# Optimization experiments

Measured on AMD Instinct MI355X. Metric: run time of the kernel, lower is better.

## Reference

```python
import jax, jax.numpy as jnp
import numpy as np

EF_DIM = 128
KNN_NUM = 8
N_POINTS = 100000


def setup_inputs() -> dict:
    key = jax.random.key(0)
    k1, k2, k3, k4, k5, k6, k7 = jax.random.split(key, 7)
    inp = jax.random.normal(k1, (N_POINTS, EF_DIM), dtype=jnp.float32)
    knn_idx = jax.random.randint(k2, (N_POINTS * KNN_NUM,), 0, N_POINTS, dtype=jnp.int64)
    knn_xyz = jax.random.normal(k3, (N_POINTS * KNN_NUM, 3), dtype=jnp.float32)
    # Linear params (stored as [in, out] so y = x @ W + b, same math as torch Linear)
    s1 = 1.0 / np.sqrt(EF_DIM + 3)
    s2 = 1.0 / np.sqrt(EF_DIM)
    W1 = jax.random.uniform(k4, (EF_DIM + 3, EF_DIM), minval=-s1, maxval=s1, dtype=jnp.float32)
    b1 = jax.random.uniform(k5, (EF_DIM,), minval=-s1, maxval=s1, dtype=jnp.float32)
    W2 = jax.random.uniform(k6, (EF_DIM, EF_DIM), minval=-s2, maxval=s2, dtype=jnp.float32)
    b2 = jax.random.uniform(k7, (EF_DIM,), minval=-s2, maxval=s2, dtype=jnp.float32)
    return {"input": inp, "KNN_idx": knn_idx, "KNN_xyz": knn_xyz,
            "W1": W1, "b1": b1, "W2": W2, "b2": b2}


def reference(input, KNN_idx, KNN_xyz, W1, b1, W2, b2):
    # Gather neighbor features: [N*K, ef_dim]
    gathered = input[KNN_idx]
    # Concat relative xyz: [N*K, ef_dim + 3]
    h = jnp.concatenate([gathered, KNN_xyz], axis=1)
    h = h @ W1 + b1
    h = jax.nn.leaky_relu(h, negative_slope=0.01)
    h = h @ W2 + b2
    # Max-pool over the KNN dimension: [N, ef_dim]
    h = h.reshape(-1, KNN_NUM, EF_DIM)
    return jnp.max(h, axis=1)
```

## Files before the change

### kernel.cpp

```cpp
#include <hip/hip_runtime.h>
#include <hip/hip_bf16.h>

#define EF 128
#define KNN 8

typedef __attribute__((ext_vector_type(8)))  short          short8;
typedef __attribute__((ext_vector_type(8)))  unsigned short ushort8;
typedef __attribute__((ext_vector_type(4)))  float          f32x4;
typedef __attribute__((ext_vector_type(16))) float          f32x16;

static __device__ __forceinline__ unsigned short f2bf(float f) {
    unsigned int x = __float_as_uint(f);
    unsigned int r = x + 0x7fffu + ((x >> 16) & 1u);
    return (unsigned short)(r >> 16);
}
static __device__ __forceinline__ short f2bf_hw(float f) {
    return (short)__bfloat16_as_ushort(__float2bfloat16(f));
}

__global__ __launch_bounds__(256) void pack_kernel(
    const float* __restrict__ W1, const float* __restrict__ W2,
    unsigned short* __restrict__ W1p, unsigned short* __restrict__ W2p)
{
    int t = blockIdx.x * 256 + threadIdx.x;
    if (t < 16384) {
        int s = t;
        int j  = s & 7;
        int l  = (s >> 3) & 63;
        int nt = (s >> 9) & 3;
        int kt = (s >> 11) & 7;
        int k = kt * 16 + (l >> 5) * 8 + j;
        int n = nt * 32 + (l & 31);
        W1p[s] = f2bf(W1[k * EF + n]);
    } else if (t < 32768) {
        int s = t - 16384;
        int j  = s & 7;
        int l  = (s >> 3) & 63;
        int nt = (s >> 9) & 7;
        int kt = (s >> 12) & 3;
        int k = kt * 32 + (l >> 4) * 8 + j;
        int n = nt * 16 + (l & 15);
        W2p[s] = f2bf(W2[k * EF + n]);
    }
}

__global__ __launch_bounds__(256) void zgemm_kernel(
    const float* __restrict__ input,
    const unsigned short* __restrict__ W1p,
    const float* __restrict__ b1,
    unsigned short* __restrict__ Z,
    int npts, int ntiles)
{
    int l = threadIdx.x & 63;
    int tile = blockIdx.x * 4 + (threadIdx.x >> 6);
    if (tile >= ntiles) return;
    int p0   = tile * 32;
    int r    = l & 31;
    int half = l >> 5;
    int prow = p0 + r;
    if (prow >= npts) prow = npts - 1;
    const float* Arow = input + (size_t)prow * EF;

    f32x16 acc[4];
#pragma unroll
    for (int nt = 0; nt < 4; ++nt)
#pragma unroll
        for (int i = 0; i < 16; ++i) acc[nt][i] = 0.f;

#pragma unroll
    for (int kt = 0; kt < 8; ++kt) {
        int k0 = kt * 16 + half * 8;
        float4 a0 = *(const float4*)(Arow + k0);
        float4 a1 = *(const float4*)(Arow + k0 + 4);
        short8 a;
        a[0] = f2bf_hw(a0.x); a[1] = f2bf_hw(a0.y);
        a[2] = f2bf_hw(a0.z); a[3] = f2bf_hw(a0.w);
        a[4] = f2bf_hw(a1.x); a[5] = f2bf_hw(a1.y);
        a[6] = f2bf_hw(a1.z); a[7] = f2bf_hw(a1.w);
#pragma unroll
        for (int nt = 0; nt < 4; ++nt) {
            short8 b = *(const short8*)(W1p + ((size_t)((kt * 4 + nt) * 64 + l)) * 8);
            acc[nt] = __builtin_amdgcn_mfma_f32_32x32x16_bf16(a, b, acc[nt], 0, 0, 0);
        }
    }

    int col = l & 31;
#pragma unroll
    for (int nt = 0; nt < 4; ++nt) {
        float bb = b1[nt * 32 + col];
#pragma unroll
        for (int reg = 0; reg < 16; ++reg) {
            int row = (reg & 3) + 8 * (reg >> 2) + 4 * half;
            int p = p0 + row;
            if (p < npts)
                Z[(size_t)p * EF + nt * 32 + col] = f2bf(acc[nt][reg] + bb);
        }
    }
}

__global__ __launch_bounds__(512) void edge_mfma_kernel(
    const unsigned short* __restrict__ Z,
    const int* __restrict__ knn_idx,
    const float* __restrict__ knn_xyz,
    const unsigned short* __restrict__ W2p,
    const float* __restrict__ W1,
    const float* __restrict__ b2,
    float* __restrict__ out,
    int npts, int nedges, int ntiles)
{
    __shared__ short8 w2lds[2048];
    __shared__ float  wlds[3 * EF];

    int l    = threadIdx.x & 63;
    int tile = blockIdx.x * 8 + (threadIdx.x >> 6);
    bool active = tile < ntiles;

    int E0 = tile * 16;
    int r  = l & 15;
    int hi = l >> 4;
    int edge = active ? (E0 + r) : 0;
    if (edge >= nedges) edge = nedges - 1;

    int   idx = knn_idx[edge];
    float x = knn_xyz[edge * 3 + 0];
    float y = knn_xyz[edge * 3 + 1];
    float z = knn_xyz[edge * 3 + 2];
    const unsigned short* Zrow = Z + (size_t)idx * EF;
    ushort8 zv[4];
#pragma unroll
    for (int kt = 0; kt < 4; ++kt)
        zv[kt] = *(const ushort8*)(Zrow + kt * 32 + hi * 8);

    {
        const short8* W2v = (const short8*)W2p;
#pragma unroll
        for (int i = threadIdx.x; i < 2048; i += 512)
            w2lds[i] = W2v[i];
        for (int t = threadIdx.x; t < 3 * EF; t += 512)
            wlds[t] = W1[EF * EF + t];
    }
    __syncthreads();
    if (!active) return;

    f32x4 acc[8];
#pragma unroll
    for (int nt = 0; nt < 8; ++nt)
#pragma unroll
        for (int i = 0; i < 4; ++i) acc[nt][i] = 0.f;

#pragma unroll
    for (int kt = 0; kt < 4; ++kt) {
        int d0 = kt * 32 + hi * 8;
        float4 wx0 = *(const float4*)&wlds[0 * EF + d0];
        float4 wx1 = *(const float4*)&wlds[0 * EF + d0 + 4];
        float4 wy0 = *(const float4*)&wlds[1 * EF + d0];
        float4 wy1 = *(const float4*)&wlds[1 * EF + d0 + 4];
        float4 wz0 = *(const float4*)&wlds[2 * EF + d0];
        float4 wz1 = *(const float4*)&wlds[2 * EF + d0 + 4];
        float wxa[8] = {wx0.x, wx0.y, wx0.z, wx0.w, wx1.x, wx1.y, wx1.z, wx1.w};
        float wya[8] = {wy0.x, wy0.y, wy0.z, wy0.w, wy1.x, wy1.y, wy1.z, wy1.w};
        float wza[8] = {wz0.x, wz0.y, wz0.z, wz0.w, wz1.x, wz1.y, wz1.z, wz1.w};

        short8 a;
#pragma unroll
        for (int j = 0; j < 8; ++j) {
            float h = __uint_as_float(((unsigned int)zv[kt][j]) << 16);
            h = fmaf(x, wxa[j], h);
            h = fmaf(y, wya[j], h);
            h = fmaf(z, wza[j], h);
            h = fmaxf(h, 0.01f * h);
            a[j] = f2bf_hw(h);
        }
#pragma unroll
        for (int nt = 0; nt < 8; ++nt) {
            short8 b = w2lds[(kt * 8 + nt) * 64 + l];
            acc[nt] = __builtin_amdgcn_mfma_f32_16x16x32_bf16(a, b, acc[nt], 0, 0, 0);
        }
    }

    int col = l & 15;
#pragma unroll
    for (int nt = 0; nt < 8; ++nt) {
        float m = fmaxf(fmaxf(acc[nt][0], acc[nt][1]),
                        fmaxf(acc[nt][2], acc[nt][3]));
        m = fmaxf(m, __shfl_xor(m, 16));
        if (!(hi & 1)) {
            int p = tile * 2 + (hi >> 1);
            if (p < npts)
                out[(size_t)p * EF + nt * 16 + col] = m + b2[nt * 16 + col];
        }
    }
}

extern "C" void kernel_launch(void* const* d_in, const int* in_sizes, int n_in,
                              void* d_out, int out_size, void* d_ws, size_t ws_size,
                              hipStream_t stream) {
    const float* input   = (const float*)d_in[0];
    const int*   knn_idx = (const int*)  d_in[1];
    const float* knn_xyz = (const float*)d_in[2];
    const float* W1      = (const float*)d_in[3];
    const float* b1      = (const float*)d_in[4];
    const float* W2      = (const float*)d_in[5];
    const float* b2      = (const float*)d_in[6];
    float*       out     = (float*)d_out;

    int npts   = in_sizes[0] / EF;
    int nedges = in_sizes[1];

    unsigned short* W1p = (unsigned short*)d_ws;
    unsigned short* W2p = W1p + 16384;
    unsigned short* Z   = (unsigned short*)((char*)d_ws + 65536);

    pack_kernel<<<128, 256, 0, stream>>>(W1, W2, W1p, W2p);

    int ztiles = (npts + 31) / 32;
    zgemm_kernel<<<(ztiles + 3) / 4, 256, 0, stream>>>(
        input, W1p, b1, Z, npts, ztiles);

    int etiles = (nedges + 15) / 16;
    edge_mfma_kernel<<<(etiles + 7) / 8, 512, 0, stream>>>(
        Z, knn_idx, knn_xyz, W2p, W1, b2, out, npts, nedges, etiles);
}
```

Baseline: 91.96 us.

## Make edge kernel persistent with double-buffered gather prefetch

The edge kernel now runs a capped grid of 1024 blocks. Each wave loops over tiles with a grid stride and prefetches the next tile's neighbor Z rows and xyz into registers while it computes the current tile. This spreads the W2/W1 LDS staging over many tiles and hides gather latency behind the MFMA work. The cost is higher register pressure from the two buffers, which may lower occupancy, and fewer waves available for latency hiding.

```diff
diff --git a/kernel.cpp b/kernel.cpp
--- a/kernel.cpp
+++ b/kernel.cpp
@@ -111,26 +111,6 @@
     __shared__ short8 w2lds[2048];
     __shared__ float  wlds[3 * EF];
 
-    int l    = threadIdx.x & 63;
-    int tile = blockIdx.x * 8 + (threadIdx.x >> 6);
-    bool active = tile < ntiles;
-
-    int E0 = tile * 16;
-    int r  = l & 15;
-    int hi = l >> 4;
-    int edge = active ? (E0 + r) : 0;
-    if (edge >= nedges) edge = nedges - 1;
-
-    int   idx = knn_idx[edge];
-    float x = knn_xyz[edge * 3 + 0];
-    float y = knn_xyz[edge * 3 + 1];
-    float z = knn_xyz[edge * 3 + 2];
-    const unsigned short* Zrow = Z + (size_t)idx * EF;
-    ushort8 zv[4];
-#pragma unroll
-    for (int kt = 0; kt < 4; ++kt)
-        zv[kt] = *(const ushort8*)(Zrow + kt * 32 + hi * 8);
-
     {
         const short8* W2v = (const short8*)W2p;
 #pragma unroll
@@ -140,55 +120,96 @@
             wlds[t] = W1[EF * EF + t];
     }
     __syncthreads();
-    if (!active) return;
-
-    f32x4 acc[8];
-#pragma unroll
-    for (int nt = 0; nt < 8; ++nt)
-#pragma unroll
-        for (int i = 0; i < 4; ++i) acc[nt][i] = 0.f;
-
-#pragma unroll
-    for (int kt = 0; kt < 4; ++kt) {
-        int d0 = kt * 32 + hi * 8;
-        float4 wx0 = *(const float4*)&wlds[0 * EF + d0];
-        float4 wx1 = *(const float4*)&wlds[0 * EF + d0 + 4];
-        float4 wy0 = *(const float4*)&wlds[1 * EF + d0];
-        float4 wy1 = *(const float4*)&wlds[1 * EF + d0 + 4];
-        float4 wz0 = *(const float4*)&wlds[2 * EF + d0];
-        float4 wz1 = *(const float4*)&wlds[2 * EF + d0 + 4];
-        float wxa[8] = {wx0.x, wx0.y, wx0.z, wx0.w, wx1.x, wx1.y, wx1.z, wx1.w};
-        float wya[8] = {wy0.x, wy0.y, wy0.z, wy0.w, wy1.x, wy1.y, wy1.z, wy1.w};
-        float wza[8] = {wz0.x, wz0.y, wz0.z, wz0.w, wz1.x, wz1.y, wz1.z, wz1.w};
-
-        short8 a;
-#pragma unroll
-        for (int j = 0; j < 8; ++j) {
-            float h = __uint_as_float(((unsigned int)zv[kt][j]) << 16);
-            h = fmaf(x, wxa[j], h);
-            h = fmaf(y, wya[j], h);
-            h = fmaf(z, wza[j], h);
-            h = fmaxf(h, 0.01f * h);
-            a[j] = f2bf_hw(h);
-        }
+
+    int l  = threadIdx.x & 63;
+    int r  = l & 15;
+    int hi = l >> 4;
+    int wid    = blockIdx.x * 8 + (threadIdx.x >> 6);
+    int stride = gridDim.x * 8;
+
+    ushort8 zvA[4], zvB[4];
+    float xA, yA, zA, xB, yB, zB;
+
+    auto fetch = [&](int tile, ushort8 (&zv)[4], float& x, float& y, float& z) {
+        int edge = tile * 16 + r;
+        if (edge >= nedges) edge = nedges - 1;
+        int idx = knn_idx[edge];
+        x = knn_xyz[edge * 3 + 0];
+        y = knn_xyz[edge * 3 + 1];
+        z = knn_xyz[edge * 3 + 2];
+        const unsigned short* Zrow = Z + (size_t)idx * EF;
+#pragma unroll
+        for (int kt = 0; kt < 4; ++kt)
+            zv[kt] = *(const ushort8*)(Zrow + kt * 32 + hi * 8);
+    };
+
+    auto compute = [&](int tile, const ushort8 (&zv)[4],
+                       float x, float y, float z) {
+        f32x4 acc[8];
+#pragma unroll
+        for (int nt = 0; nt < 8; ++nt)
+#pragma unroll
+            for (int i = 0; i < 4; ++i) acc[nt][i] = 0.f;
+
+#pragma unroll
+        for (int kt = 0; kt < 4; ++kt) {
+            int d0 = kt * 32 + hi * 8;
+            float4 wx0 = *(const float4*)&wlds[0 * EF + d0];
+            float4 wx1 = *(const float4*)&wlds[0 * EF + d0 + 4];
+            float4 wy0 = *(const float4*)&wlds[1 * EF + d0];
+            float4 wy1 = *(const float4*)&wlds[1 * EF + d0 + 4];
+            float4 wz0 = *(const float4*)&wlds[2 * EF + d0];
+            float4 wz1 = *(const float4*)&wlds[2 * EF + d0 + 4];
+            float wxa[8] = {wx0.x, wx0.y, wx0.z, wx0.w, wx1.x, wx1.y, wx1.z, wx1.w};
+            float wya[8] = {wy0.x, wy0.y, wy0.z, wy0.w, wy1.x, wy1.y, wy1.z, wy1.w};
+            float wza[8] = {wz0.x, wz0.y, wz0.z, wz0.w, wz1.x, wz1.y, wz1.z, wz1.w};
+
+            short8 a;
+#pragma unroll
+            for (int j = 0; j < 8; ++j) {
+                float h = __uint_as_float(((unsigned int)zv[kt][j]) << 16);
+                h = fmaf(x, wxa[j], h);
+                h = fmaf(y, wya[j], h);
+                h = fmaf(z, wza[j], h);
+                h = fmaxf(h, 0.01f * h);
+                a[j] = f2bf_hw(h);
+            }
+#pragma unroll
+            for (int nt = 0; nt < 8; ++nt) {
+                short8 b = w2lds[(kt * 8 + nt) * 64 + l];
+                acc[nt] = __builtin_amdgcn_mfma_f32_16x16x32_bf16(a, b, acc[nt], 0, 0, 0);
+            }
+        }
+
+        int col = l & 15;
 #pragma unroll
         for (int nt = 0; nt < 8; ++nt) {
-            short8 b = w2lds[(kt * 8 + nt) * 64 + l];
-            acc[nt] = __builtin_amdgcn_mfma_f32_16x16x32_bf16(a, b, acc[nt], 0, 0, 0);
-        }
-    }
-
-    int col = l & 15;
-#pragma unroll
-    for (int nt = 0; nt < 8; ++nt) {
-        float m = fmaxf(fmaxf(acc[nt][0], acc[nt][1]),
-                        fmaxf(acc[nt][2], acc[nt][3]));
-        m = fmaxf(m, __shfl_xor(m, 16));
-        if (!(hi & 1)) {
-            int p = tile * 2 + (hi >> 1);
-            if (p < npts)
-                out[(size_t)p * EF + nt * 16 + col] = m + b2[nt * 16 + col];
-        }
+            float m = fmaxf(fmaxf(acc[nt][0], acc[nt][1]),
+                            fmaxf(acc[nt][2], acc[nt][3]));
+            m = fmaxf(m, __shfl_xor(m, 16));
+            if (!(hi & 1)) {
+                int p = tile * 2 + (hi >> 1);
+                if (p < npts)
+                    out[(size_t)p * EF + nt * 16 + col] = m + b2[nt * 16 + col];
+            }
+        }
+    };
+
+    int t = wid;
+    if (t >= ntiles) return;
+    fetch(t, zvA, xA, yA, zA);
+    while (true) {
+        int tn = t + stride;
+        bool more = tn < ntiles;
+        if (more) fetch(tn, zvB, xB, yB, zB);
+        compute(t, zvA, xA, yA, zA);
+        if (!more) break;
+        int tnn = tn + stride;
+        bool more2 = tnn < ntiles;
+        if (more2) fetch(tnn, zvA, xA, yA, zA);
+        compute(tn, zvB, xB, yB, zB);
+        if (!more2) break;
+        t = tnn;
     }
 }
 
@@ -218,6 +239,8 @@
         input, W1p, b1, Z, npts, ztiles);
 
     int etiles = (nedges + 15) / 16;
-    edge_mfma_kernel<<<(etiles + 7) / 8, 512, 0, stream>>>(
+    int eblocks = (etiles + 7) / 8;
+    if (eblocks > 1024) eblocks = 1024;
+    edge_mfma_kernel<<<eblocks, 512, 0, stream>>>(
         Z, knn_idx, knn_xyz, W2p, W1, b2, out, npts, nedges, etiles);
 }
```

Result: slower. 235.6 us (+156.2%).

## Process two edge tiles per wave and keep xyz weights in registers as bf16

Applied to the files above, without the earlier changes.

Each wave in the edge kernel now handles 32 edges (two 16-edge MFMA tiles) instead of 16. This halves the number of blocks and reuses each W2 LDS fragment for two MFMAs. The xyz rows of W1 are no longer staged through LDS; each lane loads them from global memory and keeps them in registers as packed bf16. The W2 LDS fill is issued before the gathers so the loads can overlap. In exchange, register pressure rises (two accumulator sets), which may lower occupancy, and rounding the xyz weights to bf16 slightly changes numerics.

```diff
diff --git a/kernel.cpp b/kernel.cpp
--- a/kernel.cpp
+++ b/kernel.cpp
@@ -16,6 +16,10 @@
 }
 static __device__ __forceinline__ short f2bf_hw(float f) {
     return (short)__bfloat16_as_ushort(__float2bfloat16(f));
+}
+static __device__ __forceinline__ unsigned int pk2bf(float a, float b) {
+    return (unsigned int)(unsigned short)f2bf_hw(a)
+         | ((unsigned int)(unsigned short)f2bf_hw(b) << 16);
 }
 
 __global__ __launch_bounds__(256) void pack_kernel(
@@ -109,85 +113,125 @@
     int npts, int nedges, int ntiles)
 {
     __shared__ short8 w2lds[2048];
-    __shared__ float  wlds[3 * EF];
-
-    int l    = threadIdx.x & 63;
+
+    {
+        const short8* W2v = (const short8*)W2p;
+#pragma unroll
+        for (int i = threadIdx.x; i < 2048; i += 512)
+            w2lds[i] = W2v[i];
+    }
+
+    int l  = threadIdx.x & 63;
+    int r  = l & 15;
+    int hi = l >> 4;
     int tile = blockIdx.x * 8 + (threadIdx.x >> 6);
     bool active = tile < ntiles;
 
-    int E0 = tile * 16;
-    int r  = l & 15;
-    int hi = l >> 4;
-    int edge = active ? (E0 + r) : 0;
-    if (edge >= nedges) edge = nedges - 1;
-
-    int   idx = knn_idx[edge];
-    float x = knn_xyz[edge * 3 + 0];
-    float y = knn_xyz[edge * 3 + 1];
-    float z = knn_xyz[edge * 3 + 2];
-    const unsigned short* Zrow = Z + (size_t)idx * EF;
-    ushort8 zv[4];
-#pragma unroll
-    for (int kt = 0; kt < 4; ++kt)
-        zv[kt] = *(const ushort8*)(Zrow + kt * 32 + hi * 8);
-
+    unsigned int wxp[4][4], wyp[4][4], wzp[4][4];
     {
-        const short8* W2v = (const short8*)W2p;
-#pragma unroll
-        for (int i = threadIdx.x; i < 2048; i += 512)
-            w2lds[i] = W2v[i];
-        for (int t = threadIdx.x; t < 3 * EF; t += 512)
-            wlds[t] = W1[EF * EF + t];
-    }
+        const float* W1x = W1 + EF * EF;
+#pragma unroll
+        for (int kt = 0; kt < 4; ++kt) {
+            int d0 = kt * 32 + hi * 8;
+            float4 xa = *(const float4*)(W1x + 0 * EF + d0);
+            float4 xb = *(const float4*)(W1x + 0 * EF + d0 + 4);
+            float4 ya = *(const float4*)(W1x + 1 * EF + d0);
+            float4 yb = *(const float4*)(W1x + 1 * EF + d0 + 4);
+            float4 za = *(const float4*)(W1x + 2 * EF + d0);
+            float4 zb = *(const float4*)(W1x + 2 * EF + d0 + 4);
+            wxp[kt][0] = pk2bf(xa.x, xa.y); wxp[kt][1] = pk2bf(xa.z, xa.w);
+            wxp[kt][2] = pk2bf(xb.x, xb.y); wxp[kt][3] = pk2bf(xb.z, xb.w);
+            wyp[kt][0] = pk2bf(ya.x, ya.y); wyp[kt][1] = pk2bf(ya.z, ya.w);
+            wyp[kt][2] = pk2bf(yb.x, yb.y); wyp[kt][3] = pk2bf(yb.z, yb.w);
+            wzp[kt][0] = pk2bf(za.x, za.y); wzp[kt][1] = pk2bf(za.z, za.w);
+            wzp[kt][2] = pk2bf(zb.x, zb.y); wzp[kt][3] = pk2bf(zb.z, zb.w);
+        }
+    }
+
+    int eA = tile * 32 + r;
+    int eB = tile * 32 + 16 + r;
+    if (!active) { eA = 0; eB = 0; }
+    if (eA >= nedges) eA = nedges - 1;
+    if (eB >= nedges) eB = nedges - 1;
+
+    int   iA = knn_idx[eA],            iB = knn_idx[eB];
+    float xA = knn_xyz[eA * 3 + 0],    xB = knn_xyz[eB * 3 + 0];
+    float yA = knn_xyz[eA * 3 + 1],    yB = knn_xyz[eB * 3 + 1];
+    float zA = knn_xyz[eA * 3 + 2],    zB = knn_xyz[eB * 3 + 2];
+    const unsigned short* ZrA = Z + (size_t)iA * EF;
+    const unsigned short* ZrB = Z + (size_t)iB * EF;
+
+    ushort8 zvA[4], zvB[4];
+#pragma unroll
+    for (int kt = 0; kt < 4; ++kt) {
+        zvA[kt] = *(const ushort8*)(ZrA + kt * 32 + hi * 8);
+        zvB[kt] = *(const ushort8*)(ZrB + kt * 32 + hi * 8);
+    }
+
     __syncthreads();
     if (!active) return;
 
-    f32x4 acc[8];
+    f32x4 acc0[8], acc1[8];
 #pragma unroll
     for (int nt = 0; nt < 8; ++nt)
 #pragma unroll
-        for (int i = 0; i < 4; ++i) acc[nt][i] = 0.f;
+        for (int i = 0; i < 4; ++i) { acc0[nt][i] = 0.f; acc1[nt][i] = 0.f; }
 
 #pragma unroll
     for (int kt = 0; kt < 4; ++kt) {
-        int d0 = kt * 32 + hi * 8;
-        float4 wx0 = *(const float4*)&wlds[0 * EF + d0];
-        float4 wx1 = *(const float4*)&wlds[0 * EF + d0 + 4];
-        float4 wy0 = *(const float4*)&wlds[1 * EF + d0];
-        float4 wy1 = *(const float4*)&wlds[1 * EF + d0 + 4];
-        float4 wz0 = *(const float4*)&wlds[2 * EF + d0];
-        float4 wz1 = *(const float4*)&wlds[2 * EF + d0 + 4];
-        float wxa[8] = {wx0.x, wx0.y, wx0.z, wx0.w, wx1.x, wx1.y, wx1.z, wx1.w};
-        float wya[8] = {wy0.x, wy0.y, wy0.z, wy0.w, wy1.x, wy1.y, wy1.z, wy1.w};
-        float wza[8] = {wz0.x, wz0.y, wz0.z, wz0.w, wz1.x, wz1.y, wz1.z, wz1.w};
-
-        short8 a;
-#pragma unroll
-        for (int j = 0; j < 8; ++j) {
-            float h = __uint_as_float(((unsigned int)zv[kt][j]) << 16);
-            h = fmaf(x, wxa[j], h);
-            h = fmaf(y, wya[j], h);
-            h = fmaf(z, wza[j], h);
-            h = fmaxf(h, 0.01f * h);
-            a[j] = f2bf_hw(h);
+        short8 a0, a1;
+#pragma unroll
+        for (int jj = 0; jj < 4; ++jj) {
+            unsigned int wxu = wxp[kt][jj];
+            unsigned int wyu = wyp[kt][jj];
+            unsigned int wzu = wzp[kt][jj];
+            float wx0 = __uint_as_float(wxu << 16);
+            float wx1 = __uint_as_float(wxu & 0xffff0000u);
+            float wy0 = __uint_as_float(wyu << 16);
+            float wy1 = __uint_as_float(wyu & 0xffff0000u);
+            float wz0 = __uint_as_float(wzu << 16);
+            float wz1 = __uint_as_float(wzu & 0xffff0000u);
+
+            float h0 = __uint_as_float(((unsigned int)zvA[kt][2 * jj + 0]) << 16);
+            float h1 = __uint_as_float(((unsigned int)zvA[kt][2 * jj + 1]) << 16);
+            h0 = fmaf(xA, wx0, h0); h1 = fmaf(xA, wx1, h1);
+            h0 = fmaf(yA, wy0, h0); h1 = fmaf(yA, wy1, h1);
+            h0 = fmaf(zA, wz0, h0); h1 = fmaf(zA, wz1, h1);
+            h0 = fmaxf(h0, 0.01f * h0); h1 = fmaxf(h1, 0.01f * h1);
+            a0[2 * jj + 0] = f2bf_hw(h0); a0[2 * jj + 1] = f2bf_hw(h1);
+
+            float g0 = __uint_as_float(((unsigned int)zvB[kt][2 * jj + 0]) << 16);
+            float g1 = __uint_as_float(((unsigned int)zvB[kt][2 * jj + 1]) << 16);
+            g0 = fmaf(xB, wx0, g0); g1 = fmaf(xB, wx1, g1);
+            g0 = fmaf(yB, wy0, g0); g1 = fmaf(yB, wy1, g1);
+            g0 = fmaf(zB, wz0, g0); g1 = fmaf(zB, wz1, g1);
+            g0 = fmaxf(g0, 0.01f * g0); g1 = fmaxf(g1, 0.01f * g1);
+            a1[2 * jj + 0] = f2bf_hw(g0); a1[2 * jj + 1] = f2bf_hw(g1);
         }
 #pragma unroll
         for (int nt = 0; nt < 8; ++nt) {
             short8 b = w2lds[(kt * 8 + nt) * 64 + l];
-            acc[nt] = __builtin_amdgcn_mfma_f32_16x16x32_bf16(a, b, acc[nt], 0, 0, 0);
+            acc0[nt] = __builtin_amdgcn_mfma_f32_16x16x32_bf16(a0, b, acc0[nt], 0, 0, 0);
+            acc1[nt] = __builtin_amdgcn_mfma_f32_16x16x32_bf16(a1, b, acc1[nt], 0, 0, 0);
         }
     }
 
     int col = l & 15;
+    int p0  = tile * 4;
 #pragma unroll
     for (int nt = 0; nt < 8; ++nt) {
-        float m = fmaxf(fmaxf(acc[nt][0], acc[nt][1]),
-                        fmaxf(acc[nt][2], acc[nt][3]));
-        m = fmaxf(m, __shfl_xor(m, 16));
+        float bb = b2[nt * 16 + col];
+        float m0 = fmaxf(fmaxf(acc0[nt][0], acc0[nt][1]),
+                         fmaxf(acc0[nt][2], acc0[nt][3]));
+        m0 = fmaxf(m0, __shfl_xor(m0, 16));
+        float m1 = fmaxf(fmaxf(acc1[nt][0], acc1[nt][1]),
+                         fmaxf(acc1[nt][2], acc1[nt][3]));
+        m1 = fmaxf(m1, __shfl_xor(m1, 16));
         if (!(hi & 1)) {
-            int p = tile * 2 + (hi >> 1);
-            if (p < npts)
-                out[(size_t)p * EF + nt * 16 + col] = m + b2[nt * 16 + col];
+            int pa = p0 + (hi >> 1);
+            int pb = p0 + 2 + (hi >> 1);
+            if (pa < npts) out[(size_t)pa * EF + nt * 16 + col] = m0 + bb;
+            if (pb < npts) out[(size_t)pb * EF + nt * 16 + col] = m1 + bb;
         }
     }
 }
@@ -217,7 +261,8 @@
     zgemm_kernel<<<(ztiles + 3) / 4, 256, 0, stream>>>(
         input, W1p, b1, Z, npts, ztiles);
 
-    int etiles = (nedges + 15) / 16;
-    edge_mfma_kernel<<<(etiles + 7) / 8, 512, 0, stream>>>(
+    int etiles = (nedges + 31) / 32;
+    int eblocks = (etiles + 7) / 8;
+    edge_mfma_kernel<<<eblocks, 512, 0, stream>>>(
         Z, knn_idx, knn_xyz, W2p, W1, b2, out, npts, nedges, etiles);
 }
```

Result: slower. 107.5 us (+16.9%).
